# Kernel tuning notes

Measured on AMD Instinct MI355X. Metric: run time of the kernel, lower is better.

The kernel has to match this reference:

```python
import jax, jax.numpy as jnp
import numpy as np

N_NODES = 100000
N_EDGES = 1000000
EMB_DIM = 64
N_LAYERS = 5
NUM_CLASS = 10
NUM_GRAPHS = 128
BN_EPS = 1e-5


def setup_inputs() -> dict:
    key = jax.random.key(0)
    ks = jax.random.split(key, 16)
    s = 0.05
    inp = {
        "x": jnp.zeros((N_NODES,), dtype=jnp.int64),
        "edge_index": jax.random.randint(ks[0], (2, N_EDGES), 0, N_NODES, dtype=jnp.int64),
        "edge_attr": jax.random.normal(ks[1], (N_EDGES, 7), dtype=jnp.float32),
        "batch": jnp.sort(jax.random.randint(ks[2], (N_NODES,), 0, NUM_GRAPHS, dtype=jnp.int64)),
        # parameters
        "node_table": jax.random.normal(ks[3], (1, EMB_DIM), dtype=jnp.float32) * s,
        "ew": jax.random.normal(ks[4], (N_LAYERS, 7, EMB_DIM), dtype=jnp.float32) * s,   # edge_encoder weight
        "eb": jax.random.normal(ks[5], (N_LAYERS, EMB_DIM), dtype=jnp.float32) * s,
        "w1": jax.random.normal(ks[6], (N_LAYERS, EMB_DIM, EMB_DIM), dtype=jnp.float32) * s,
        "b1": jax.random.normal(ks[7], (N_LAYERS, EMB_DIM), dtype=jnp.float32) * s,
        "w2": jax.random.normal(ks[8], (N_LAYERS, EMB_DIM, EMB_DIM), dtype=jnp.float32) * s,
        "b2": jax.random.normal(ks[9], (N_LAYERS, EMB_DIM), dtype=jnp.float32) * s,
        "gamma": jnp.ones((N_LAYERS, EMB_DIM), dtype=jnp.float32),
        "beta": jnp.zeros((N_LAYERS, EMB_DIM), dtype=jnp.float32),
        "pw": jax.random.normal(ks[10], (EMB_DIM, NUM_CLASS), dtype=jnp.float32) * s,
        "pb": jnp.zeros((NUM_CLASS,), dtype=jnp.float32),
    }
    return inp


def reference(x, edge_index, edge_attr, batch, node_table, ew, eb, w1, b1, w2, b2, gamma, beta, pw, pb):
    n = x.shape[0]
    src, dst = edge_index[0], edge_index[1]
    h = node_table[x]  # [N, D] node embedding lookup (all index 0)
    for l in range(N_LAYERS):
        edge_emb = edge_attr @ ew[l] + eb[l]                      # [E, D]
        msg = jax.nn.relu(h[src] + edge_emb)                      # gather + add + relu
        agg = jax.ops.segment_sum(msg, dst, num_segments=n)       # scatter-add
        z = h + agg                                               # (1 + eps)*x with eps=0
        z = jax.nn.relu(z @ w1[l] + b1[l]) @ w2[l] + b2[l]        # GIN MLP
        mu = z.mean(axis=0)
        var = z.var(axis=0)                                       # biased var, matches BN training
        z = (z - mu) * jax.lax.rsqrt(var + BN_EPS) * gamma[l] + beta[l]
        if l != N_LAYERS - 1:
            z = jax.nn.relu(z)                                    # dropout is identity (eval)
        h = z
    # global mean pool over graphs
    sums = jax.ops.segment_sum(h, batch, num_segments=NUM_GRAPHS)           # [B, D]
    cnt = jax.ops.segment_sum(jnp.ones((n,), h.dtype), batch, num_segments=NUM_GRAPHS)
    h_graph = sums / jnp.maximum(cnt, 1.0)[:, None]
    return h_graph @ pw + pb
```

## Files before the change

kernel.cpp:

```cpp
#include <hip/hip_runtime.h>


__global__ void hist_k(const int* __restrict__ dst, int* __restrict__ cnt, int E) {
  int stride = gridDim.x * blockDim.x;
  for (int i = blockIdx.x * blockDim.x + threadIdx.x; i < E; i += stride)
    atomicAdd(&cnt[dst[i]], 1);
}

__global__ void scan_a_k(const int* __restrict__ deg, int* __restrict__ rowptr,
                         int* __restrict__ bsum, int n) {
  __shared__ int s[256];
  int i = blockIdx.x * 256 + threadIdx.x;
  int v = (i < n) ? deg[i] : 0;
  s[threadIdx.x] = v;
  __syncthreads();
  for (int off = 1; off < 256; off <<= 1) {
    int t = (threadIdx.x >= off) ? s[threadIdx.x - off] : 0;
    __syncthreads();
    s[threadIdx.x] += t;
    __syncthreads();
  }
  if (i < n) rowptr[i] = s[threadIdx.x] - v;
  if (threadIdx.x == 255) bsum[blockIdx.x] = s[255];
}

__global__ void scan_b_k(int* __restrict__ bsum, int nb) {
  __shared__ int s[512];
  int t = threadIdx.x;
  int v = (t < nb) ? bsum[t] : 0;
  s[t] = v;
  __syncthreads();
  for (int off = 1; off < 512; off <<= 1) {
    int u = (t >= off) ? s[t - off] : 0;
    __syncthreads();
    s[t] += u;
    __syncthreads();
  }
  if (t < nb) bsum[t] = s[t] - v;
}

__global__ void scan_c_k(int* __restrict__ rowptr, int* __restrict__ cur,
                         const int* __restrict__ bsum, int n, int E) {
  int i = blockIdx.x * 256 + threadIdx.x;
  if (i < n) {
    int r = rowptr[i] + bsum[blockIdx.x];
    rowptr[i] = r;
    cur[i] = r;
  }
  if (i == 0) rowptr[n] = E;
}

__global__ void scatter_k(const int* __restrict__ src, const int* __restrict__ dst,
                          int* __restrict__ cur, float* __restrict__ sea,
                          const float* __restrict__ ea, int E) {
  int stride = gridDim.x * blockDim.x;
  for (int i = blockIdx.x * blockDim.x + threadIdx.x; i < E; i += stride) {
    int d = dst[i];
    int pos = atomicAdd(&cur[d], 1);
    const float* a = ea + (size_t)i * 7;
    float4 lo = make_float4(a[0], a[1], a[2], a[3]);
    float4 hi = make_float4(a[4], a[5], a[6], __int_as_float(src[i]));
    float4* o = (float4*)(sea + (size_t)pos * 8);
    o[0] = lo;
    o[1] = hi;
  }
}

#define NPW 8
template<int MODE>
__global__ __launch_bounds__(256)
void agg_k(const float* __restrict__ hprev, const int* __restrict__ x,
           const float* __restrict__ ntab, const int* __restrict__ rowptr,
           const float* __restrict__ sea, const float* __restrict__ ewl,
           const float* __restrict__ ebl, const float* __restrict__ statsP,
           const float* __restrict__ gamP, const float* __restrict__ betP,
           float* __restrict__ zout, int n) {
  int wv = (blockIdx.x * blockDim.x + threadIdx.x) >> 6;
  int lane = threadIdx.x & 63;
  int g0 = wv * NPW;
  if (g0 >= n) return;
  int gend = g0 + NPW; if (gend > n) gend = n;

  float ew_[7];
#pragma unroll
  for (int k = 0; k < 7; k++) ew_[k] = ewl[k * 64 + lane];
  float ebv = ebl[lane];

  float cnst = 0.f, sc = 1.f, sh = 0.f;
  if (MODE == 0) cnst = ntab[lane];
  if (MODE == 2) {
    float s1 = statsP[lane], s2 = statsP[64 + lane];
    float mu = s1 / (float)n;
    float var = s2 / (float)n - mu * mu;
    sc = gamP[lane] * rsqrtf(var + 1e-5f);
    sh = betP[lane] - mu * sc;
  }

  auto raw_ld = [&](int row) -> float {
    if (MODE == 0) return 0.f;
    if (MODE == 1) {
      int xv = __builtin_amdgcn_readfirstlane(x[row]);
      return ntab[(size_t)xv * 64 + lane];
    }
    return hprev[(size_t)row * 64 + lane];
  };
  auto finish_h = [&](float v) -> float {
    if (MODE == 0) return cnst;
    if (MODE == 1) return v;
    return fmaxf(fmaf(v, sc, sh), 0.f);
  };

  int P1 = __builtin_amdgcn_readfirstlane(rowptr[gend]);
  int p0 = __builtin_amdgcn_readfirstlane(rowptr[g0]);
  int nd = g0;
  int pn = __builtin_amdgcn_readfirstlane(rowptr[nd + 1]);
  float selfv = raw_ld(nd);
  float acc = 0.f;

  for (int p = p0; p < P1; p += 8) {
    const float* R[8];
    int s[8];
#pragma unroll
    for (int u = 0; u < 8; u++) {
      int t = p + u;
      int q = t < P1 ? t : P1 - 1;
      R[u] = sea + (size_t)q * 8;
      s[u] = __builtin_amdgcn_readfirstlane(__float_as_int(R[u][7]));
    }
    float h[8];
#pragma unroll
    for (int u = 0; u < 8; u++) h[u] = (MODE == 0) ? cnst : raw_ld(s[u]);
    float m[8];
#pragma unroll
    for (int u = 0; u < 8; u++) m[u] = ebv;
#pragma unroll
    for (int k = 0; k < 7; k++) {
#pragma unroll
      for (int u = 0; u < 8; u++) m[u] = fmaf(R[u][k], ew_[k], m[u]);
    }
#pragma unroll
    for (int u = 0; u < 8; u++) {
      if (p + u < P1) {
        while (p + u >= pn) {
          zout[(size_t)nd * 64 + lane] = finish_h(selfv) + acc;
          nd++;
          selfv = raw_ld(nd);
          pn = __builtin_amdgcn_readfirstlane(rowptr[nd + 1]);
          acc = 0.f;
        }
        acc += fmaxf(finish_h(h[u]) + m[u], 0.f);
      }
    }
  }
  while (nd < gend) {
    zout[(size_t)nd * 64 + lane] = finish_h(selfv) + acc;
    nd++;
    acc = 0.f;
    if (nd < gend) selfv = raw_ld(nd);
  }
}

#define ASTR 132
__global__ __launch_bounds__(256, 3)
void mlp_k(const float* __restrict__ zin, const float* __restrict__ w1l,
           const float* __restrict__ b1l, const float* __restrict__ w2l,
           const float* __restrict__ b2l, float* __restrict__ zout,
           float* __restrict__ statslot, int n) {
  __shared__ float As[64 * ASTR];
  __shared__ float Ws[4096];
  __shared__ float red[128];
  int tid = threadIdx.x;
  int tx = tid & 15, ty = tid >> 4;
  if (tid < 128) red[tid] = 0.f;
  int r0 = blockIdx.x * 128;

  float4 w2r[4];
  {
    const float4* wb = (const float4*)w2l;
#pragma unroll
    for (int it = 0; it < 4; it++) w2r[it] = wb[it * 256 + tid];
  }

  {
    const float4* gz = (const float4*)(zin + (size_t)r0 * 64);
#pragma unroll
    for (int it = 0; it < 8; it++) {
      int f4 = it * 256 + tid;
      int row = f4 >> 4, kq = f4 & 15;
      float4 v = make_float4(0.f, 0.f, 0.f, 0.f);
      if (r0 + row < n) v = gz[f4];
      As[(4 * kq + 0) * ASTR + row] = v.x;
      As[(4 * kq + 1) * ASTR + row] = v.y;
      As[(4 * kq + 2) * ASTR + row] = v.z;
      As[(4 * kq + 3) * ASTR + row] = v.w;
    }
    const float4* wa = (const float4*)w1l;
    float4* wd = (float4*)Ws;
#pragma unroll
    for (int it = 0; it < 4; it++) wd[it * 256 + tid] = wa[it * 256 + tid];
  }
  __syncthreads();

  const float4 b1v = *(const float4*)(b1l + tx * 4);
  float t[8][4];
#pragma unroll
  for (int rr = 0; rr < 8; rr++) {
    t[rr][0] = b1v.x; t[rr][1] = b1v.y; t[rr][2] = b1v.z; t[rr][3] = b1v.w;
  }
#pragma unroll 8
  for (int k = 0; k < 64; k++) {
    float4 aA = *(const float4*)&As[k * ASTR + ty * 8];
    float4 aB = *(const float4*)&As[k * ASTR + ty * 8 + 4];
    float4 b = *(const float4*)&Ws[k * 64 + tx * 4];
    float a[8] = {aA.x, aA.y, aA.z, aA.w, aB.x, aB.y, aB.z, aB.w};
#pragma unroll
    for (int rr = 0; rr < 8; rr++) {
      t[rr][0] = fmaf(a[rr], b.x, t[rr][0]);
      t[rr][1] = fmaf(a[rr], b.y, t[rr][1]);
      t[rr][2] = fmaf(a[rr], b.z, t[rr][2]);
      t[rr][3] = fmaf(a[rr], b.w, t[rr][3]);
    }
  }
  __syncthreads();

#pragma unroll
  for (int cc = 0; cc < 4; cc++)
#pragma unroll
    for (int rr = 0; rr < 8; rr++)
      As[(tx * 4 + cc) * ASTR + ty * 8 + rr] = fmaxf(t[rr][cc], 0.f);
  {
    float4* wd = (float4*)Ws;
#pragma unroll
    for (int it = 0; it < 4; it++) wd[it * 256 + tid] = w2r[it];
  }
  __syncthreads();

  const float4 b2v = *(const float4*)(b2l + tx * 4);
  float o[8][4];
#pragma unroll
  for (int rr = 0; rr < 8; rr++) {
    o[rr][0] = b2v.x; o[rr][1] = b2v.y; o[rr][2] = b2v.z; o[rr][3] = b2v.w;
  }
#pragma unroll 8
  for (int k = 0; k < 64; k++) {
    float4 aA = *(const float4*)&As[k * ASTR + ty * 8];
    float4 aB = *(const float4*)&As[k * ASTR + ty * 8 + 4];
    float4 b = *(const float4*)&Ws[k * 64 + tx * 4];
    float a[8] = {aA.x, aA.y, aA.z, aA.w, aB.x, aB.y, aB.z, aB.w};
#pragma unroll
    for (int rr = 0; rr < 8; rr++) {
      o[rr][0] = fmaf(a[rr], b.x, o[rr][0]);
      o[rr][1] = fmaf(a[rr], b.y, o[rr][1]);
      o[rr][2] = fmaf(a[rr], b.z, o[rr][2]);
      o[rr][3] = fmaf(a[rr], b.w, o[rr][3]);
    }
  }

  float s1[4] = {0.f, 0.f, 0.f, 0.f}, s2[4] = {0.f, 0.f, 0.f, 0.f};
#pragma unroll
  for (int rr = 0; rr < 8; rr++) {
    int grow = r0 + ty * 8 + rr;
    if (grow < n) {
      float4 v = make_float4(o[rr][0], o[rr][1], o[rr][2], o[rr][3]);
      *(float4*)(zout + (size_t)grow * 64 + tx * 4) = v;
#pragma unroll
      for (int cc = 0; cc < 4; cc++) {
        s1[cc] += o[rr][cc];
        s2[cc] = fmaf(o[rr][cc], o[rr][cc], s2[cc]);
      }
    }
  }
#pragma unroll
  for (int cc = 0; cc < 4; cc++) {
    s1[cc] += __shfl_xor(s1[cc], 16); s1[cc] += __shfl_xor(s1[cc], 32);
    s2[cc] += __shfl_xor(s2[cc], 16); s2[cc] += __shfl_xor(s2[cc], 32);
  }
  if ((tid & 48) == 0) {
#pragma unroll
    for (int cc = 0; cc < 4; cc++) {
      atomicAdd(&red[tx * 4 + cc], s1[cc]);
      atomicAdd(&red[64 + tx * 4 + cc], s2[cc]);
    }
  }
  __syncthreads();
  if (tid < 128) atomicAdd(&statslot[tid], red[tid]);
}

__global__ void pool_k(const float* __restrict__ z2, const float* __restrict__ stats,
                       const float* __restrict__ gam, const float* __restrict__ bet,
                       const int* __restrict__ batch, float* __restrict__ gsum,
                       float* __restrict__ gcnt, int n, int ch) {
  int wid = (blockIdx.x * blockDim.x + threadIdx.x) >> 6;
  int lane = threadIdx.x & 63;
  int v0 = wid * ch;
  if (v0 >= n) return;
  int v1 = v0 + ch; if (v1 > n) v1 = n;
  float st1 = stats[lane], st2 = stats[64 + lane];
  float mu = st1 / (float)n;
  float var = st2 / (float)n - mu * mu;
  float sc = gam[lane] * rsqrtf(var + 1e-5f);
  float sh = bet[lane] - mu * sc;
  int curb = batch[v0];
  float acc = 0.f;
  int cnt = 0;
  for (int v = v0; v < v1; v++) {
    int b = batch[v];
    if (b != curb) {
      atomicAdd(&gsum[curb * 64 + lane], acc);
      if (lane == 0) atomicAdd(&gcnt[curb], (float)cnt);
      acc = 0.f; cnt = 0; curb = b;
    }
    acc += fmaf(z2[(size_t)v * 64 + lane], sc, sh);
    cnt++;
  }
  atomicAdd(&gsum[curb * 64 + lane], acc);
  if (lane == 0) atomicAdd(&gcnt[curb], (float)cnt);
}

__global__ void head_k(const float* __restrict__ gsum, const float* __restrict__ gcnt,
                       const float* __restrict__ pw, const float* __restrict__ pb,
                       float* __restrict__ out, int B, int C) {
  for (int idx = threadIdx.x; idx < B * C; idx += blockDim.x) {
    int g = idx / C, c = idx % C;
    float inv = 1.f / fmaxf(gcnt[g], 1.f);
    float s = pb[c];
    for (int d = 0; d < 64; d++)
      s = fmaf(gsum[g * 64 + d] * inv, pw[d * C + c], s);
    out[idx] = s;
  }
}

extern "C" void kernel_launch(void* const* d_in, const int* in_sizes, int n_in,
                              void* d_out, int out_size, void* d_ws, size_t ws_size,
                              hipStream_t stream) {
  const int*   x     = (const int*)d_in[0];
  const int*   ei    = (const int*)d_in[1];
  const float* ea    = (const float*)d_in[2];
  const int*   batch = (const int*)d_in[3];
  const float* ntab  = (const float*)d_in[4];
  const float* ew    = (const float*)d_in[5];
  const float* eb    = (const float*)d_in[6];
  const float* w1    = (const float*)d_in[7];
  const float* b1    = (const float*)d_in[8];
  const float* w2    = (const float*)d_in[9];
  const float* b2    = (const float*)d_in[10];
  const float* gamma = (const float*)d_in[11];
  const float* beta  = (const float*)d_in[12];
  const float* pw    = (const float*)d_in[13];
  const float* pb    = (const float*)d_in[14];
  float* out = (float*)d_out;

  int N = in_sizes[0];
  int E = in_sizes[1] / 2;
  int L = in_sizes[6] / 64;
  int C = in_sizes[14];
  int B = out_size / C;
  bool tab1 = (in_sizes[4] == 64);

  const int* src = ei;
  const int* dst = ei + E;

  char* ws = (char*)d_ws;
  auto alloc = [&](size_t bytes) -> char* {
    char* p = ws;
    ws += (bytes + 255) & ~(size_t)255;
    return p;
  };
  float* hbuf    = (float*)alloc((size_t)N * 64 * 4);
  float* tbuf    = (float*)alloc((size_t)N * 64 * 4);
  int*   rowptr  = (int*)alloc((size_t)(N + 1) * 4);
  int*   cur     = (int*)alloc((size_t)N * 4);
  float* sea     = (float*)alloc((size_t)(E + 16) * 8 * 4);
  int*   bsum    = (int*)alloc(512 * 4);
  float* bnstats = (float*)alloc((size_t)L * 128 * 4);
  float* gsum    = (float*)alloc((size_t)B * 64 * 4);
  float* gcnt    = (float*)alloc((size_t)B * 4);

  hipMemsetAsync(cur, 0, (size_t)N * 4, stream);
  hipMemsetAsync(bnstats, 0, (size_t)L * 128 * 4, stream);
  hipMemsetAsync(gsum, 0, (size_t)B * 64 * 4, stream);
  hipMemsetAsync(gcnt, 0, (size_t)B * 4, stream);

  hist_k<<<2048, 256, 0, stream>>>(dst, cur, E);
  int NB = (N + 255) / 256;
  scan_a_k<<<NB, 256, 0, stream>>>(cur, rowptr, bsum, N);
  scan_b_k<<<1, 512, 0, stream>>>(bsum, NB);
  scan_c_k<<<NB, 256, 0, stream>>>(rowptr, cur, bsum, N, E);
  scatter_k<<<4096, 256, 0, stream>>>(src, dst, cur, sea, ea, E);

  int aggWaves = (N + NPW - 1) / NPW;
  int aggBlocks = (aggWaves * 64 + 255) / 256;
  int mlpBlocks = (N + 127) / 128;
  for (int l = 0; l < L; l++) {
    const float* ewl = ew + (size_t)l * 448;
    const float* ebl = eb + (size_t)l * 64;
    const float* stP = bnstats + (size_t)(l > 0 ? l - 1 : 0) * 128;
    const float* gmP = gamma + (size_t)(l > 0 ? l - 1 : 0) * 64;
    const float* btP = beta + (size_t)(l > 0 ? l - 1 : 0) * 64;
    if (l == 0) {
      if (tab1)
        agg_k<0><<<aggBlocks, 256, 0, stream>>>(hbuf, x, ntab, rowptr, sea, ewl,
                                                ebl, stP, gmP, btP, tbuf, N);
      else
        agg_k<1><<<aggBlocks, 256, 0, stream>>>(hbuf, x, ntab, rowptr, sea, ewl,
                                                ebl, stP, gmP, btP, tbuf, N);
    } else {
      agg_k<2><<<aggBlocks, 256, 0, stream>>>(hbuf, x, ntab, rowptr, sea, ewl,
                                              ebl, stP, gmP, btP, tbuf, N);
    }
    mlp_k<<<mlpBlocks, 256, 0, stream>>>(tbuf, w1 + (size_t)l * 4096,
                                         b1 + (size_t)l * 64,
                                         w2 + (size_t)l * 4096,
                                         b2 + (size_t)l * 64,
                                         hbuf, bnstats + (size_t)l * 128, N);
  }

  int ch = 64;
  int poolWaves = (N + ch - 1) / ch;
  int poolBlocks = (poolWaves + 3) / 4;
  pool_k<<<poolBlocks, 256, 0, stream>>>(hbuf,
                                         bnstats + (size_t)(L - 1) * 128,
                                         gamma + (size_t)(L - 1) * 64,
                                         beta + (size_t)(L - 1) * 64,
                                         batch, gsum, gcnt, N, ch);
  head_k<<<1, 256, 0, stream>>>(gsum, gcnt, pw, pb, out, B, C);
}
```

Before: 637.3 us.

## Software-pipeline edge gather loads and read MLP weights directly from global

The edge aggregation loop now issues the edge-attribute and source-feature loads for the next group of 8 edges before reducing the current group, so memory latency overlaps with accumulation. Separately, the MLP kernel drops its shared-memory weight tile and reads W1/W2 straight from global (relying on cache), freeing 16KB of LDS and raising the occupancy hint to 4 blocks. The risks are higher register pressure from the prefetched stage, and slower weight access since each k-step now does a global load instead of an LDS read.

New measurement: 757.3 us. +18.8%, slower.

```diff
diff --git a/kernel.cpp b/kernel.cpp
--- a/kernel.cpp
+++ b/kernel.cpp
@@ -117,27 +117,30 @@
   float selfv = raw_ld(nd);
   float acc = 0.f;
 
+#define STAGE(P, M, H)                                                         \
+  {                                                                            \
+    _Pragma("unroll")                                                          \
+    for (int u = 0; u < 8; u++) {                                              \
+      int t_ = (P) + u;                                                        \
+      int q_ = t_ < P1 ? t_ : P1 - 1;                                          \
+      const float* Rr_ = sea + (size_t)q_ * 8;                                 \
+      float mm_ = ebv;                                                         \
+      mm_ = fmaf(Rr_[0], ew_[0], mm_); mm_ = fmaf(Rr_[1], ew_[1], mm_);        \
+      mm_ = fmaf(Rr_[2], ew_[2], mm_); mm_ = fmaf(Rr_[3], ew_[3], mm_);        \
+      mm_ = fmaf(Rr_[4], ew_[4], mm_); mm_ = fmaf(Rr_[5], ew_[5], mm_);        \
+      mm_ = fmaf(Rr_[6], ew_[6], mm_);                                         \
+      M[u] = mm_;                                                              \
+      int sid_ = __builtin_amdgcn_readfirstlane(__float_as_int(Rr_[7]));       \
+      H[u] = (MODE == 0) ? cnst : raw_ld(sid_);                                \
+    }                                                                          \
+  }
+
+  float mC[8], hC[8];
+  if (p0 < P1) STAGE(p0, mC, hC);
   for (int p = p0; p < P1; p += 8) {
-    const float* R[8];
-    int s[8];
-#pragma unroll
-    for (int u = 0; u < 8; u++) {
-      int t = p + u;
-      int q = t < P1 ? t : P1 - 1;
-      R[u] = sea + (size_t)q * 8;
-      s[u] = __builtin_amdgcn_readfirstlane(__float_as_int(R[u][7]));
-    }
-    float h[8];
-#pragma unroll
-    for (int u = 0; u < 8; u++) h[u] = (MODE == 0) ? cnst : raw_ld(s[u]);
-    float m[8];
-#pragma unroll
-    for (int u = 0; u < 8; u++) m[u] = ebv;
-#pragma unroll
-    for (int k = 0; k < 7; k++) {
-#pragma unroll
-      for (int u = 0; u < 8; u++) m[u] = fmaf(R[u][k], ew_[k], m[u]);
-    }
+    float mN[8], hN[8];
+    bool more = (p + 8 < P1);
+    if (more) STAGE(p + 8, mN, hN);
 #pragma unroll
     for (int u = 0; u < 8; u++) {
       if (p + u < P1) {
@@ -148,10 +151,13 @@
           pn = __builtin_amdgcn_readfirstlane(rowptr[nd + 1]);
           acc = 0.f;
         }
-        acc += fmaxf(finish_h(h[u]) + m[u], 0.f);
+        acc += fmaxf(finish_h(hC[u]) + mC[u], 0.f);
       }
     }
-  }
+#pragma unroll
+    for (int u = 0; u < 8; u++) { mC[u] = mN[u]; hC[u] = hN[u]; }
+  }
+#undef STAGE
   while (nd < gend) {
     zout[(size_t)nd * 64 + lane] = finish_h(selfv) + acc;
     nd++;
@@ -161,25 +167,17 @@
 }
 
 #define ASTR 132
-__global__ __launch_bounds__(256, 3)
+__global__ __launch_bounds__(256, 4)
 void mlp_k(const float* __restrict__ zin, const float* __restrict__ w1l,
            const float* __restrict__ b1l, const float* __restrict__ w2l,
            const float* __restrict__ b2l, float* __restrict__ zout,
            float* __restrict__ statslot, int n) {
   __shared__ float As[64 * ASTR];
-  __shared__ float Ws[4096];
   __shared__ float red[128];
   int tid = threadIdx.x;
   int tx = tid & 15, ty = tid >> 4;
   if (tid < 128) red[tid] = 0.f;
   int r0 = blockIdx.x * 128;
-
-  float4 w2r[4];
-  {
-    const float4* wb = (const float4*)w2l;
-#pragma unroll
-    for (int it = 0; it < 4; it++) w2r[it] = wb[it * 256 + tid];
-  }
 
   {
     const float4* gz = (const float4*)(zin + (size_t)r0 * 64);
@@ -194,10 +192,6 @@
       As[(4 * kq + 2) * ASTR + row] = v.z;
       As[(4 * kq + 3) * ASTR + row] = v.w;
     }
-    const float4* wa = (const float4*)w1l;
-    float4* wd = (float4*)Ws;
-#pragma unroll
-    for (int it = 0; it < 4; it++) wd[it * 256 + tid] = wa[it * 256 + tid];
   }
   __syncthreads();
 
@@ -211,7 +205,7 @@
   for (int k = 0; k < 64; k++) {
     float4 aA = *(const float4*)&As[k * ASTR + ty * 8];
     float4 aB = *(const float4*)&As[k * ASTR + ty * 8 + 4];
-    float4 b = *(const float4*)&Ws[k * 64 + tx * 4];
+    float4 b = *(const float4*)(w1l + k * 64 + tx * 4);
     float a[8] = {aA.x, aA.y, aA.z, aA.w, aB.x, aB.y, aB.z, aB.w};
 #pragma unroll
     for (int rr = 0; rr < 8; rr++) {
@@ -228,11 +222,6 @@
 #pragma unroll
     for (int rr = 0; rr < 8; rr++)
       As[(tx * 4 + cc) * ASTR + ty * 8 + rr] = fmaxf(t[rr][cc], 0.f);
-  {
-    float4* wd = (float4*)Ws;
-#pragma unroll
-    for (int it = 0; it < 4; it++) wd[it * 256 + tid] = w2r[it];
-  }
   __syncthreads();
 
   const float4 b2v = *(const float4*)(b2l + tx * 4);
@@ -245,7 +234,7 @@
   for (int k = 0; k < 64; k++) {
     float4 aA = *(const float4*)&As[k * ASTR + ty * 8];
     float4 aB = *(const float4*)&As[k * ASTR + ty * 8 + 4];
-    float4 b = *(const float4*)&Ws[k * 64 + tx * 4];
+    float4 b = *(const float4*)(w2l + k * 64 + tx * 4);
     float a[8] = {aA.x, aA.y, aA.z, aA.w, aB.x, aB.y, aB.z, aB.w};
 #pragma unroll
     for (int rr = 0; rr < 8; rr++) {
```
